# Optimization experiments

Hardware: AMD Instinct MI355X
Metric: run time of the kernel (lower is better)

## Reference

```python
import jax, jax.numpy as jnp
import numpy as np

N_NODES = 100000
N_EDGES = 3200000
D_FEAT = 128


def setup_inputs() -> dict:
    key = jax.random.key(0)
    k1, k2, k3, k4 = jax.random.split(key, 4)
    edge_row = jax.random.randint(k1, (N_EDGES,), 0, N_NODES)
    edge_col = jax.random.randint(k2, (N_EDGES,), 0, N_NODES)
    edge_val = jax.random.uniform(k3, (N_EDGES,), dtype=jnp.float32)
    embs = jax.random.normal(k4, (N_NODES, D_FEAT), dtype=jnp.float32)
    return {
        "edge_row": edge_row,
        "edge_col": edge_col,
        "edge_val": edge_val,
        "embs": embs,
        "n_nodes": N_NODES,
    }


def reference(edge_row, edge_col, edge_val, embs, n_nodes):
    # out[r] = sum_{e: row[e]==r} val[e] * embs[col[e]]  == (sparse adj) @ embs
    msgs = embs[edge_col] * edge_val[:, None]  # [E, D] gather + scale
    return jax.ops.segment_sum(msgs, edge_row, num_segments=n_nodes)  # [N, D]
```

## Files before the change

### kernel.cpp

```cpp
#include <hip/hip_runtime.h>
#include <hip/hip_fp16.h>


#define D_FEAT 128
#define CSHIFT 9
#define CROWS 512
#define MAXNBC 256
#define PAD 16
#define BLK1 256
#define EPT1 16
#define EPB1 (BLK1 * EPT1)
#define BLK2 1024

__device__ __forceinline__ int wave_incl_scan(int x, int lane) {
#pragma unroll
    for (int off = 1; off < 64; off <<= 1) {
        int y = __shfl_up(x, off, 64);
        if (lane >= off) x += y;
    }
    return x;
}

__global__ __launch_bounds__(BLK1) void k_part1(const int* __restrict__ row,
                                                const int* __restrict__ col,
                                                const float* __restrict__ val,
                                                int* __restrict__ gcur,
                                                int2* __restrict__ tmp1,
                                                int n_edges, int nbc, int slot) {
    __shared__ int2 stage[EPB1];
    __shared__ int lcnt[MAXNBC], lstart[257], lcur[MAXNBC];
    __shared__ int lbase[MAXNBC], lroom[MAXNBC];
    __shared__ int wsum[4];
    int tid = threadIdx.x, lane = tid & 63, wid = tid >> 6;
    for (int j = tid; j < nbc; j += BLK1) { lcnt[j] = 0; lcur[j] = 0; }
    __syncthreads();

    int base = blockIdx.x * EPB1;
    int ne = n_edges - base; if (ne > EPB1) ne = EPB1;

    int r[EPT1], c[EPT1]; float v[EPT1];
#pragma unroll
    for (int k = 0; k < EPT1; ++k) {
        int e = base + k * BLK1 + tid;
        r[k] = -1;
        if (e < n_edges) {
            r[k] = row[e]; c[k] = col[e]; v[k] = val[e];
            atomicAdd(&lcnt[r[k] >> CSHIFT], 1);
        }
    }
    __syncthreads();
    int cv = (tid < nbc) ? lcnt[tid] : 0;
    int incl = wave_incl_scan(cv, lane);
    if (lane == 63) wsum[wid] = incl;
    __syncthreads();
    if (tid < 4) {
        int w = wsum[tid];
        int ss = w;
#pragma unroll
        for (int off = 1; off < 4; off <<= 1) {
            int y = __shfl_up(ss, off, 64);
            if (tid >= off) ss += y;
        }
        wsum[tid] = ss - w;
    }
    __syncthreads();
    int ex = wsum[wid] + incl - cv;
    lstart[tid] = (tid < nbc) ? ex : ne;
    if (tid == BLK1 - 1) lstart[256] = ne;
    if (tid < nbc && cv) {
        int res = atomicAdd(&gcur[tid * PAD], cv);
        lbase[tid] = tid * slot + res;
        lroom[tid] = slot - res;
    }
    __syncthreads();
    if (tid == 0 && nbc < 256) lstart[nbc] = ne;
    __syncthreads();
#pragma unroll
    for (int k = 0; k < EPT1; ++k) {
        if (r[k] >= 0) {
            int b = r[k] >> CSHIFT;
            int sl = lstart[b] + atomicAdd(&lcur[b], 1);
            stage[sl] = make_int2(((r[k] & (CROWS - 1)) << 17) | c[k],
                                  __float_as_int(v[k]));
        }
    }
    __syncthreads();
#define P1_SEARCH_STORE(ii)                                                \
    {                                                                      \
        int _i = (ii);                                                     \
        int lo = 0;                                                        \
        lo += (lstart[lo + 128] <= _i) ? 128 : 0;                          \
        lo += (lstart[lo + 64]  <= _i) ? 64  : 0;                          \
        lo += (lstart[lo + 32]  <= _i) ? 32  : 0;                          \
        lo += (lstart[lo + 16]  <= _i) ? 16  : 0;                          \
        lo += (lstart[lo + 8]   <= _i) ? 8   : 0;                          \
        lo += (lstart[lo + 4]   <= _i) ? 4   : 0;                          \
        lo += (lstart[lo + 2]   <= _i) ? 2   : 0;                          \
        lo += (lstart[lo + 1]   <= _i) ? 1   : 0;                          \
        int off = _i - lstart[lo];                                         \
        if (off < lroom[lo])   \
            tmp1[lbase[lo] + off] = stage[_i];                             \
    }
    if (ne == EPB1) {
#pragma unroll 4
        for (int k = 0; k < EPT1; ++k) P1_SEARCH_STORE(k * BLK1 + tid);
    } else {
        for (int i = tid; i < ne; i += BLK1) P1_SEARCH_STORE(i);
    }
#undef P1_SEARCH_STORE
}

__global__ __launch_bounds__(BLK2) void k_p2conv(const int2* __restrict__ tmp1,
                                                 const int* __restrict__ gcur,
                                                 int2* __restrict__ pcv,
                                                 int* __restrict__ row_start,
                                                 int* __restrict__ row_cnt,
                                                 int n_nodes, int nbc, int slot,
                                                 const float* __restrict__ embs,
                                                 __half* __restrict__ embs16,
                                                 int n_units) {
    int tid = threadIdx.x;
    if ((int)blockIdx.x >= nbc) {
        int i = (blockIdx.x - nbc) * BLK2 + tid;
        if (i >= n_units) return;
        const float4* src = reinterpret_cast<const float4*>(embs) + (size_t)i * 2;
        float4 f0 = src[0];
        float4 f1 = src[1];
        __half2* dst = reinterpret_cast<__half2*>(embs16) + (size_t)i * 4;
        dst[0] = __floats2half2_rn(f0.x, f0.y);
        dst[1] = __floats2half2_rn(f0.z, f0.w);
        dst[2] = __floats2half2_rn(f1.x, f1.y);
        dst[3] = __floats2half2_rn(f1.z, f1.w);
        return;
    }
    __shared__ int rcnt[CROWS], rstart[CROWS], rcur[CROWS];
    __shared__ int wsum[8];
    __shared__ int s[256];
    int b = blockIdx.x;
    int lane = tid & 63, wid = tid >> 6;

    if (tid < 256) {
        int c = (tid < nbc) ? gcur[tid * PAD] : 0;
        s[tid] = (c > slot) ? slot : c;
    }
    __syncthreads();
    for (int off = 1; off < 256; off <<= 1) {
        int u = (tid < 256 && tid >= off) ? s[tid - off] : 0;
        __syncthreads();
        if (tid < 256) s[tid] += u;
        __syncthreads();
    }
    int cnt = gcur[b * PAD]; if (cnt > slot) cnt = slot;
    int pbase = s[b] - cnt;
    const int2* src = tmp1 + (size_t)b * slot;

    for (int j = tid; j < CROWS; j += BLK2) { rcnt[j] = 0; rcur[j] = 0; }
    __syncthreads();
    for (int i = tid; i < cnt; i += BLK2)
        atomicAdd(&rcnt[((unsigned)src[i].x) >> 17], 1);
    __syncthreads();
    int v = (tid < CROWS) ? rcnt[tid] : 0;
    int incl = wave_incl_scan(v, lane);
    if (lane == 63 && wid < 8) wsum[wid] = incl;
    __syncthreads();
    if (tid < 8) {
        int w = wsum[tid];
        int ss = w;
#pragma unroll
        for (int off = 1; off < 8; off <<= 1) {
            int y = __shfl_up(ss, off, 64);
            if (tid >= off) ss += y;
        }
        wsum[tid] = ss - w;
    }
    __syncthreads();
    if (tid < CROWS) rstart[tid] = wsum[wid] + incl - v;
    __syncthreads();
    if (tid < CROWS) {
        int gr = (b << CSHIFT) + tid;
        if (gr < n_nodes) {
            row_start[gr] = pbase + rstart[tid];
            row_cnt[gr]   = v;
        }
    }
    for (int i = tid; i < cnt; i += BLK2) {
        int2 p = src[i];
        int lr = ((unsigned)p.x) >> 17;
        int pos = pbase + rstart[lr] + atomicAdd(&rcur[lr], 1);
        pcv[pos] = make_int2(p.x & 0x1FFFF, p.y);
    }
}

__global__ __launch_bounds__(256) void k_rows_h(const int2* __restrict__ pcv,
                                                const int* __restrict__ row_start,
                                                const int* __restrict__ row_cnt,
                                                const __half2* __restrict__ eb,
                                                float* __restrict__ out,
                                                int r_begin, int r_end) {
    int gtid = blockIdx.x * blockDim.x + threadIdx.x;
    int r = r_begin + (gtid >> 6);
    int lane = threadIdx.x & 63;
    if (r >= r_end) return;

    int start = row_start[r];
    int end   = start + row_cnt[r];

    float2 acc = make_float2(0.f, 0.f);

    int i = start;
    for (; i + 8 <= end; i += 8) {
        int2 p[8];
#pragma unroll
        for (int k = 0; k < 8; ++k) p[k] = pcv[i + k];
        __half2 h[8];
#pragma unroll
        for (int k = 0; k < 8; ++k) h[k] = eb[(size_t)p[k].x * 64 + lane];
#pragma unroll
        for (int k = 0; k < 8; ++k) {
            float v = __int_as_float(p[k].y);
            float2 f = __half22float2(h[k]);
            acc.x += v * f.x;
            acc.y += v * f.y;
        }
    }
    for (; i < end; ++i) {
        int2 p = pcv[i];
        float v = __int_as_float(p.y);
        float2 f = __half22float2(eb[(size_t)p.x * 64 + lane]);
        acc.x += v * f.x;
        acc.y += v * f.y;
    }
    reinterpret_cast<float2*>(out)[(size_t)r * 64 + lane] = acc;
}

__global__ void gcn_scatter_atomic(const int* __restrict__ edge_row,
                                   const int* __restrict__ edge_col,
                                   const float* __restrict__ edge_val,
                                   const float* __restrict__ embs,
                                   float* __restrict__ out, int n_edges) {
    long long tid = (long long)blockIdx.x * blockDim.x + threadIdx.x;
    int sub = (int)(tid & 31);
    long long edge = tid >> 5;
    if (edge >= n_edges) return;
    int r = edge_row[edge];
    int c = edge_col[edge];
    float v = edge_val[edge];
    const float4* src = reinterpret_cast<const float4*>(embs + (size_t)c * D_FEAT);
    float4 m = src[sub];
    float* dst = out + (size_t)r * D_FEAT + (size_t)sub * 4;
    atomicAdd(dst + 0, m.x * v);
    atomicAdd(dst + 1, m.y * v);
    atomicAdd(dst + 2, m.z * v);
    atomicAdd(dst + 3, m.w * v);
}

extern "C" void kernel_launch(void* const* d_in, const int* in_sizes, int n_in,
                              void* d_out, int out_size, void* d_ws, size_t ws_size,
                              hipStream_t stream) {
    const int*   edge_row = (const int*)d_in[0];
    const int*   edge_col = (const int*)d_in[1];
    const float* edge_val = (const float*)d_in[2];
    const float* embs     = (const float*)d_in[3];
    float*       out      = (float*)d_out;

    const int n_edges = in_sizes[0];
    const int n_nodes = out_size / D_FEAT;
    const int nbc = (n_nodes + CROWS - 1) >> CSHIFT;

    const int avg = (n_edges + nbc - 1) / nbc;
    const int slot = (avg + (avg >> 2) + 2048 + 63) & ~63;

    char* ws = (char*)d_ws;
    const size_t off_pcv       = 0;
    const size_t off_row_start = off_pcv + (size_t)n_edges * 8;
    const size_t off_row_cnt   = off_row_start + (size_t)n_nodes * 4;
    const size_t off_gcur      = off_row_cnt + (size_t)n_nodes * 4;
    const size_t off_embs16    = off_gcur + (size_t)MAXNBC * PAD * 4;
    const size_t full_ws       = off_embs16 + (size_t)n_nodes * D_FEAT * 2;

    bool tmp_fits = ((size_t)nbc * slot * 8 <= (size_t)out_size * 4);
    bool packs_ok = (n_nodes <= 131072) && (nbc <= MAXNBC);

    if (ws_size < full_ws || !tmp_fits || !packs_ok) {
        hipMemsetAsync(d_out, 0, (size_t)out_size * sizeof(float), stream);
        long long total = (long long)n_edges * 32;
        int blocks = (int)((total + 255) / 256);
        gcn_scatter_atomic<<<blocks, 256, 0, stream>>>(edge_row, edge_col, edge_val,
                                                       embs, out, n_edges);
        return;
    }

    int2*   pcv       = (int2*)(ws + off_pcv);
    int*    row_start = (int*)(ws + off_row_start);
    int*    row_cnt   = (int*)(ws + off_row_cnt);
    int*    gcur      = (int*)(ws + off_gcur);
    __half* embs16    = (__half*)(ws + off_embs16);
    int2*   tmp1      = (int2*)d_out;

    hipMemsetAsync(gcur, 0, (size_t)MAXNBC * PAD * 4, stream);

    const int nchunks = (n_edges + EPB1 - 1) / EPB1;
    const int n_units = n_nodes * (D_FEAT / 8);
    const int conv_blocks = (n_units + BLK2 - 1) / BLK2;

    k_part1<<<nchunks, BLK1, 0, stream>>>(edge_row, edge_col, edge_val,
                                          gcur, tmp1, n_edges, nbc, slot);
    k_p2conv<<<nbc + conv_blocks, BLK2, 0, stream>>>(
        tmp1, gcur, pcv, row_start, row_cnt, n_nodes, nbc, slot,
        embs, embs16, n_units);

    int half = (n_nodes + 1) / 2;
    for (int k = 0; k < 2; ++k) {
        int r0 = k * half;
        int r1 = r0 + half; if (r1 > n_nodes) r1 = n_nodes;
        if (r1 <= r0) continue;
        long long thr = (long long)(r1 - r0) * 64;
        int blocks = (int)((thr + 255) / 256);
        k_rows_h<<<blocks, 256, 0, stream>>>(pcv, row_start, row_cnt,
                                             (const __half2*)embs16, out, r0, r1);
    }
}
```

Baseline: 310.2 us.

## Move fp16 embedding conversion into partition kernel and merge row launches

The fp32-to-fp16 embedding conversion blocks now ride along with the first edge-partition kernel instead of the second pass, and each conversion thread handles 16 floats. The second pass becomes a pure per-bucket sort. The two half-range row-aggregation launches are replaced by a single launch over all rows. The aim is to overlap the conversion with the partition stage's atomics-heavy work and to drop one launch. The conversion blocks may now compete for CUs with the partition blocks, which use a lot of shared memory.

```diff
diff --git a/kernel.cpp b/kernel.cpp
--- a/kernel.cpp
+++ b/kernel.cpp
@@ -21,17 +21,41 @@
     return x;
 }
 
-__global__ __launch_bounds__(BLK1) void k_part1(const int* __restrict__ row,
-                                                const int* __restrict__ col,
-                                                const float* __restrict__ val,
-                                                int* __restrict__ gcur,
-                                                int2* __restrict__ tmp1,
-                                                int n_edges, int nbc, int slot) {
+__global__ __launch_bounds__(BLK1) void k_part1conv(const int* __restrict__ row,
+                                                    const int* __restrict__ col,
+                                                    const float* __restrict__ val,
+                                                    int* __restrict__ gcur,
+                                                    int2* __restrict__ tmp1,
+                                                    int n_edges, int nbc, int slot,
+                                                    int nchunks,
+                                                    const float* __restrict__ embs,
+                                                    __half* __restrict__ embs16,
+                                                    int n_units16) {
+    int tid = threadIdx.x;
+    if ((int)blockIdx.x >= nchunks) {
+        int i = (blockIdx.x - nchunks) * BLK1 + tid;
+        if (i >= n_units16) return;
+        const float4* src = reinterpret_cast<const float4*>(embs) + (size_t)i * 4;
+        float4 f0 = src[0];
+        float4 f1 = src[1];
+        float4 f2 = src[2];
+        float4 f3 = src[3];
+        __half2* dst = reinterpret_cast<__half2*>(embs16) + (size_t)i * 8;
+        dst[0] = __floats2half2_rn(f0.x, f0.y);
+        dst[1] = __floats2half2_rn(f0.z, f0.w);
+        dst[2] = __floats2half2_rn(f1.x, f1.y);
+        dst[3] = __floats2half2_rn(f1.z, f1.w);
+        dst[4] = __floats2half2_rn(f2.x, f2.y);
+        dst[5] = __floats2half2_rn(f2.z, f2.w);
+        dst[6] = __floats2half2_rn(f3.x, f3.y);
+        dst[7] = __floats2half2_rn(f3.z, f3.w);
+        return;
+    }
     __shared__ int2 stage[EPB1];
     __shared__ int lcnt[MAXNBC], lstart[257], lcur[MAXNBC];
     __shared__ int lbase[MAXNBC], lroom[MAXNBC];
     __shared__ int wsum[4];
-    int tid = threadIdx.x, lane = tid & 63, wid = tid >> 6;
+    int lane = tid & 63, wid = tid >> 6;
     for (int j = tid; j < nbc; j += BLK1) { lcnt[j] = 0; lcur[j] = 0; }
     __syncthreads();
 
@@ -110,33 +134,16 @@
 #undef P1_SEARCH_STORE
 }
 
-__global__ __launch_bounds__(BLK2) void k_p2conv(const int2* __restrict__ tmp1,
-                                                 const int* __restrict__ gcur,
-                                                 int2* __restrict__ pcv,
-                                                 int* __restrict__ row_start,
-                                                 int* __restrict__ row_cnt,
-                                                 int n_nodes, int nbc, int slot,
-                                                 const float* __restrict__ embs,
-                                                 __half* __restrict__ embs16,
-                                                 int n_units) {
-    int tid = threadIdx.x;
-    if ((int)blockIdx.x >= nbc) {
-        int i = (blockIdx.x - nbc) * BLK2 + tid;
-        if (i >= n_units) return;
-        const float4* src = reinterpret_cast<const float4*>(embs) + (size_t)i * 2;
-        float4 f0 = src[0];
-        float4 f1 = src[1];
-        __half2* dst = reinterpret_cast<__half2*>(embs16) + (size_t)i * 4;
-        dst[0] = __floats2half2_rn(f0.x, f0.y);
-        dst[1] = __floats2half2_rn(f0.z, f0.w);
-        dst[2] = __floats2half2_rn(f1.x, f1.y);
-        dst[3] = __floats2half2_rn(f1.z, f1.w);
-        return;
-    }
+__global__ __launch_bounds__(BLK2) void k_p2(const int2* __restrict__ tmp1,
+                                             const int* __restrict__ gcur,
+                                             int2* __restrict__ pcv,
+                                             int* __restrict__ row_start,
+                                             int* __restrict__ row_cnt,
+                                             int n_nodes, int nbc, int slot) {
     __shared__ int rcnt[CROWS], rstart[CROWS], rcur[CROWS];
     __shared__ int wsum[8];
     __shared__ int s[256];
-    int b = blockIdx.x;
+    int b = blockIdx.x, tid = threadIdx.x;
     int lane = tid & 63, wid = tid >> 6;
 
     if (tid < 256) {
@@ -195,12 +202,11 @@
                                                 const int* __restrict__ row_start,
                                                 const int* __restrict__ row_cnt,
                                                 const __half2* __restrict__ eb,
-                                                float* __restrict__ out,
-                                                int r_begin, int r_end) {
+                                                float* __restrict__ out, int n_nodes) {
     int gtid = blockIdx.x * blockDim.x + threadIdx.x;
-    int r = r_begin + (gtid >> 6);
+    int r = gtid >> 6;
     int lane = threadIdx.x & 63;
-    if (r >= r_end) return;
+    if (r >= n_nodes) return;
 
     int start = row_start[r];
     int end   = start + row_cnt[r];
@@ -279,7 +285,8 @@
     const size_t full_ws       = off_embs16 + (size_t)n_nodes * D_FEAT * 2;
 
     bool tmp_fits = ((size_t)nbc * slot * 8 <= (size_t)out_size * 4);
-    bool packs_ok = (n_nodes <= 131072) && (nbc <= MAXNBC);
+    bool packs_ok = (n_nodes <= 131072) && (nbc <= MAXNBC) &&
+                    ((n_nodes * D_FEAT) % 16 == 0);
 
     if (ws_size < full_ws || !tmp_fits || !packs_ok) {
         hipMemsetAsync(d_out, 0, (size_t)out_size * sizeof(float), stream);
@@ -300,23 +307,17 @@
     hipMemsetAsync(gcur, 0, (size_t)MAXNBC * PAD * 4, stream);
 
     const int nchunks = (n_edges + EPB1 - 1) / EPB1;
-    const int n_units = n_nodes * (D_FEAT / 8);
-    const int conv_blocks = (n_units + BLK2 - 1) / BLK2;
-
-    k_part1<<<nchunks, BLK1, 0, stream>>>(edge_row, edge_col, edge_val,
-                                          gcur, tmp1, n_edges, nbc, slot);
-    k_p2conv<<<nbc + conv_blocks, BLK2, 0, stream>>>(
-        tmp1, gcur, pcv, row_start, row_cnt, n_nodes, nbc, slot,
-        embs, embs16, n_units);
-
-    int half = (n_nodes + 1) / 2;
-    for (int k = 0; k < 2; ++k) {
-        int r0 = k * half;
-        int r1 = r0 + half; if (r1 > n_nodes) r1 = n_nodes;
-        if (r1 <= r0) continue;
-        long long thr = (long long)(r1 - r0) * 64;
-        int blocks = (int)((thr + 255) / 256);
-        k_rows_h<<<blocks, 256, 0, stream>>>(pcv, row_start, row_cnt,
-                                             (const __half2*)embs16, out, r0, r1);
-    }
-}
+    const int n_units16 = n_nodes * (D_FEAT / 16);
+    const int conv_blocks = (n_units16 + BLK1 - 1) / BLK1;
+
+    k_part1conv<<<nchunks + conv_blocks, BLK1, 0, stream>>>(
+        edge_row, edge_col, edge_val, gcur, tmp1, n_edges, nbc, slot,
+        nchunks, embs, embs16, n_units16);
+    k_p2<<<nbc, BLK2, 0, stream>>>(tmp1, gcur, pcv, row_start, row_cnt,
+                                   n_nodes, nbc, slot);
+
+    long long rows_threads = (long long)n_nodes * 64;
+    int rblocks = (int)((rows_threads + 255) / 256);
+    k_rows_h<<<rblocks, 256, 0, stream>>>(pcv, row_start, row_cnt,
+                                          (const __half2*)embs16, out, n_nodes);
+}
```

New measurement: 300.6 us (median of 2 runs). -3.1%, faster.
